# Kernel tuning notes

Measured on AMD Instinct MI355X. Metric: run time of the kernel, lower is better.

Reference implementation:

```python
import jax, jax.numpy as jnp
import numpy as np

N_TYPES = 4
D_DESC = 256
H = 256
N_ATOMS = 131072


def setup_inputs() -> dict:
    key = jax.random.key(0)
    ks = jax.random.split(key, 8)
    descriptors = jax.random.normal(ks[0], (N_ATOMS, D_DESC), dtype=jnp.float32)
    elems = jax.random.randint(ks[1], (N_ATOMS,), 0, N_TYPES, dtype=jnp.int32)
    # Per-type MLP params: stacked over the type axis T.
    s1 = 1.0 / np.sqrt(D_DESC)
    s2 = 1.0 / np.sqrt(H)
    W1 = jax.random.normal(ks[2], (N_TYPES, D_DESC, H), dtype=jnp.float32) * s1
    b1 = jnp.zeros((N_TYPES, H), dtype=jnp.float32)
    W2 = jax.random.normal(ks[3], (N_TYPES, H, H), dtype=jnp.float32) * s2
    b2 = jnp.zeros((N_TYPES, H), dtype=jnp.float32)
    W3 = jax.random.normal(ks[4], (N_TYPES, H), dtype=jnp.float32) * s2  # output dim 1, squeezed
    b3 = jnp.zeros((N_TYPES,), dtype=jnp.float32)
    return {"descriptors": descriptors, "elems": elems,
            "W1": W1, "b1": b1, "W2": W2, "b2": b2, "W3": W3, "b3": b3}


def reference(descriptors, elems, W1, b1, W2, b2, W3, b3):
    # Equivalent to: for each atom, run the MLP subnet of its element type and
    # scatter the scalar output back to the per-atom attribute vector.
    # Vectorized as batched-per-type GEMMs followed by a per-atom type gather
    # (dense dispatch: fixed shapes, jit-friendly).
    # h1: [T, N, H]
    h1 = jnp.tanh(jnp.einsum('nd,tdh->tnh', descriptors, W1) + b1[:, None, :])
    h2 = jnp.tanh(jnp.einsum('tnh,thk->tnk', h1, W2) + b2[:, None, :])
    out_t = jnp.einsum('tnh,th->tn', h2, W3) + b3[:, None]  # [T, N]
    # select per-atom row according to its element type
    per_atom = out_t[elems, jnp.arange(out_t.shape[1])]  # [N]
    return per_atom
```

## Files before the change

### kernel.cpp

```cpp
#include <hip/hip_runtime.h>
#include <hip/hip_bf16.h>
#include <stdint.h>


typedef __attribute__((ext_vector_type(8))) short short8;
typedef __attribute__((ext_vector_type(4))) float f32x4;

#define NPB 256
#define NTY 4
#define XBUF_BYTES 69632

typedef __attribute__((address_space(3))) void lds_void;
typedef __attribute__((address_space(1))) const void glb_void;

__device__ __forceinline__ unsigned short f2bf(float f) {
    union { float f; uint32_t u; } v; v.f = f;
    uint32_t u = v.u;
    uint32_t r = (u + 0x7FFFu + ((u >> 16) & 1u)) >> 16;
    return (unsigned short)r;
}
__device__ __forceinline__ float fast_tanh(float x) {
    x = fminf(fmaxf(x, -10.0f), 10.0f);
    float e = __expf(2.0f * x);
    return (e - 1.0f) * __builtin_amdgcn_rcpf(e + 1.0f);
}


__global__ void count_k(const int* __restrict__ elems, int n, int chunk,
                        int* __restrict__ counts) {
    __shared__ int h[NTY];
    if (threadIdx.x < NTY) h[threadIdx.x] = 0;
    __syncthreads();
    const int start = blockIdx.x * chunk;
    const int end   = min(start + chunk, n);
    for (int i = start + threadIdx.x; i < end; i += blockDim.x)
        atomicAdd(&h[elems[i]], 1);
    __syncthreads();
    if (threadIdx.x < NTY) counts[threadIdx.x * NPB + blockIdx.x] = h[threadIdx.x];
}

__global__ void prefix_k(const int* __restrict__ counts,
                         int* __restrict__ cursor, int* __restrict__ hdr) {
    __shared__ int tot[NTY];
    const int t = threadIdx.x;
    if (t < NTY) {
        int s = 0;
        for (int b = 0; b < NPB; ++b) s += counts[t * NPB + b];
        tot[t] = s;
    }
    __syncthreads();
    if (t == 0) {
        int b = 0, tb = 0;
        for (int ty = 0; ty < NTY; ++ty) {
            hdr[ty]      = tot[ty];
            hdr[8 + ty]  = b;
            hdr[12 + ty] = tb;
            b  += tot[ty];
            tb += (tot[ty] + 63) >> 6;
        }
        hdr[16] = tb;
    }
    __syncthreads();
    if (t < NTY) {
        int run = hdr[8 + t];
        for (int b = 0; b < NPB; ++b) {
            cursor[t * NPB + b] = run;
            run += counts[t * NPB + b];
        }
    }
}

__global__ void scatter_k(const int* __restrict__ elems, int n, int chunk,
                          const int* __restrict__ cursor, int* __restrict__ sorted) {
    __shared__ int cur[NTY];
    if (threadIdx.x < NTY) cur[threadIdx.x] = cursor[threadIdx.x * NPB + blockIdx.x];
    __syncthreads();
    const int start = blockIdx.x * chunk;
    const int end   = min(start + chunk, n);
    for (int i = start + threadIdx.x; i < end; i += blockDim.x) {
        int ty  = elems[i];
        int pos = atomicAdd(&cur[ty], 1);
        sorted[pos] = i;
    }
}

__global__ void wconv_k(const float* __restrict__ W1, const float* __restrict__ W2,
                        unsigned short* __restrict__ w1s, unsigned short* __restrict__ w2s) {
    int gid  = blockIdx.x * blockDim.x + threadIdx.x;
    int lane = gid & 63;
    int ks   = (gid >> 6) & 7;
    int tile = (gid >> 9) & 15;
    int t    = (gid >> 13) & 3;
    int layer = gid >> 15;
    const float* W = layer ? W2 : W1;
    unsigned short* o = layer ? w2s : w1s;
    int dbase = ks * 32 + ((lane >> 4) << 3);
    int col   = tile * 16 + (lane & 15);
    unsigned short v[8];
#pragma unroll
    for (int j = 0; j < 8; ++j)
        v[j] = f2bf(W[(size_t)t * 65536 + (size_t)(dbase + j) * 256 + col]);
    unsigned short* dst = o + ((size_t)(t * 16 + tile) * 8 + ks) * 512 + lane * 8;
    *(short8*)dst = *(short8*)v;
}

__device__ __forceinline__ short8 read_xfrag(const char* cb, int a, int c0) {
    const int swz = (a & 7) << 4;
    const int cs0 = c0 ^ swz;
    const int cs1 = (c0 + 16) ^ swz;
    const int ab  = (a >> 4) * 17408 + (a & 15) * 64;
    const float4 f0 = *(const float4*)(cb + ab + (cs0 >> 6) * 1088 + (cs0 & 0x30));
    const float4 f1 = *(const float4*)(cb + ab + (cs1 >> 6) * 1088 + (cs1 & 0x30));
    union { short8 s; __hip_bfloat162 h[4]; } u;
    u.h[0] = __float22bfloat162_rn(make_float2(f0.x, f0.y));
    u.h[1] = __float22bfloat162_rn(make_float2(f0.z, f0.w));
    u.h[2] = __float22bfloat162_rn(make_float2(f1.x, f1.y));
    u.h[3] = __float22bfloat162_rn(make_float2(f1.z, f1.w));
    return u.s;
}

__global__ __launch_bounds__(512, 2) void mlp_k(
    const float* __restrict__ desc,
    const float* __restrict__ b1g,
    const float* __restrict__ b2g,
    const float* __restrict__ W3,
    const float* __restrict__ b3,
    const int* __restrict__ hdr,
    const int* __restrict__ sorted,
    const unsigned short* __restrict__ w1s,
    const unsigned short* __restrict__ w2s,
    float* __restrict__ out)
{
    __shared__ __align__(16) char buf[2][XBUF_BYTES];
    __shared__ float part[8][64];

    const int tid  = threadIdx.x;
    const int lane = tid & 63;
    const int w    = tid >> 6;
    const int g    = lane >> 4;
    const int a16  = lane & 15;
    const int sa   = lane >> 2;
    const int qq   = lane & 3;
    const int gw   = w & 3;
    const int ch   = w >> 2;
    const int sswz = (sa & 7) << 4;

    const int t     = blockIdx.x >> 6;
    const int bslot = blockIdx.x & 63;
    const int cnt   = hdr[t];
    const int base  = hdr[8 + t];
    const int ntile = (cnt + 63) >> 6;
    if (bslot >= ntile) return;

#define STAGE(J, BP)                                                          \
    {                                                                         \
        const int gg_  = (J) * 64 + gw * 16 + sa;                             \
        const int idx_ = (gg_ < cnt) ? sorted[base + gg_] : 0;                \
        const float* rowp_ = desc + (size_t)idx_ * 256;                       \
        _Pragma("unroll")                                                     \
        for (int i_ = 0; i_ < 8; ++i_) {                                      \
            const int c_ = ch * 8 + i_;                                       \
            const float* src_ = rowp_ + (((c_ * 64 + qq * 16) ^ sswz) >> 2);  \
            char* dst_ = (BP) + gw * 17408 + c_ * 1088;                       \
            __builtin_amdgcn_global_load_lds((glb_void*)src_,                 \
                                             (lds_void*)dst_, 16, 0, 0);      \
        }                                                                     \
    }

    int j = bslot;
    STAGE(j, buf[0]);

    const unsigned short* w1t = w1s + (size_t)t * (16 * 8 * 512);
    const unsigned short* w2t = w2s + (size_t)t * (16 * 8 * 512);
    short8 wf1[2][8], wf2[2][8];
#pragma unroll
    for (int q = 0; q < 2; ++q)
#pragma unroll
        for (int ks = 0; ks < 8; ++ks) {
            wf1[q][ks] = *(const short8*)(w1t + ((size_t)((w * 2 + q) * 8 + ks)) * 512 + lane * 8);
            wf2[q][ks] = *(const short8*)(w2t + ((size_t)((w * 2 + q) * 8 + ks)) * 512 + lane * 8);
        }
    float4 bq[2];
    float  w3r[2], b2r[2];
#pragma unroll
    for (int q = 0; q < 2; ++q) {
        bq[q]  = *(const float4*)(b1g + t * 256 + (w * 2 + q) * 16 + g * 4);
        const int kout = (w * 2 + q) * 16 + a16;
        w3r[q] = W3[t * 256 + kout];
        b2r[q] = b2g[t * 256 + kout];
    }
    const float b3v = b3[t];

    for (int k = 0;; ++k) {
        const int cur = k & 1;
        const int jn  = j + 64;
        const bool has_next = (jn < ntile);

        asm volatile("s_waitcnt vmcnt(0)" ::: "memory");
        __syncthreads();

        if (has_next) STAGE(jn, buf[cur ^ 1]);

        const char* cb = buf[cur];

        f32x4 acc[2][4];
#pragma unroll
        for (int q = 0; q < 2; ++q)
#pragma unroll
            for (int nt = 0; nt < 4; ++nt)
                acc[q][nt] = (f32x4){0.f, 0.f, 0.f, 0.f};

#pragma unroll
        for (int ks = 0; ks < 8; ++ks) {
            short8 bh[4];
            const int c0 = ks * 128 + g * 32;
#pragma unroll
            for (int nt = 0; nt < 4; ++nt)
                bh[nt] = read_xfrag(cb, nt * 16 + a16, c0);
#pragma unroll
            for (int q = 0; q < 2; ++q)
#pragma unroll
                for (int nt = 0; nt < 4; ++nt)
                    acc[q][nt] = __builtin_amdgcn_mfma_f32_16x16x32_bf16(wf1[q][ks], bh[nt], acc[q][nt], 0, 0, 0);
        }
        __syncthreads();

        {
            char* hb = buf[cur];
#pragma unroll
            for (int q = 0; q < 2; ++q) {
                const int h0 = (w * 2 + q) * 16 + g * 4;
#pragma unroll
                for (int nt = 0; nt < 4; ++nt) {
                    const int atom = nt * 16 + a16;
                    unsigned short h4[4];
                    h4[0] = f2bf(fast_tanh(acc[q][nt][0] + bq[q].x));
                    h4[1] = f2bf(fast_tanh(acc[q][nt][1] + bq[q].y));
                    h4[2] = f2bf(fast_tanh(acc[q][nt][2] + bq[q].z));
                    h4[3] = f2bf(fast_tanh(acc[q][nt][3] + bq[q].w));
                    const int off = atom * 512 + ((h0 * 2) ^ ((atom & 7) << 4));
                    *(ushort4*)(hb + off) = *(ushort4*)h4;
                }
            }
        }
        __syncthreads();

        f32x4 acc2[4][2];
#pragma unroll
        for (int mt = 0; mt < 4; ++mt)
#pragma unroll
            for (int q = 0; q < 2; ++q)
                acc2[mt][q] = (f32x4){0.f, 0.f, 0.f, 0.f};

#pragma unroll
        for (int ks = 0; ks < 8; ++ks) {
            short8 ah[4];
            const int colb = ks * 64 + g * 16;
#pragma unroll
            for (int mt = 0; mt < 4; ++mt) {
                const int row = mt * 16 + a16;
                const int off = row * 512 + (colb ^ ((row & 7) << 4));
                ah[mt] = *(const short8*)(cb + off);
            }
#pragma unroll
            for (int mt = 0; mt < 4; ++mt)
#pragma unroll
                for (int q = 0; q < 2; ++q)
                    acc2[mt][q] = __builtin_amdgcn_mfma_f32_16x16x32_bf16(ah[mt], wf2[q][ks], acc2[mt][q], 0, 0, 0);
        }

        float psum[4][4];
#pragma unroll
        for (int mt = 0; mt < 4; ++mt)
#pragma unroll
            for (int r = 0; r < 4; ++r)
                psum[mt][r] = 0.f;

#pragma unroll
        for (int q = 0; q < 2; ++q)
#pragma unroll
            for (int mt = 0; mt < 4; ++mt)
#pragma unroll
                for (int r = 0; r < 4; ++r)
                    psum[mt][r] += fast_tanh(acc2[mt][q][r] + b2r[q]) * w3r[q];

#pragma unroll
        for (int m = 1; m <= 8; m <<= 1)
#pragma unroll
            for (int mt = 0; mt < 4; ++mt)
#pragma unroll
                for (int r = 0; r < 4; ++r)
                    psum[mt][r] += __shfl_xor(psum[mt][r], m, 64);

        if (a16 == 0) {
#pragma unroll
            for (int mt = 0; mt < 4; ++mt)
#pragma unroll
                for (int r = 0; r < 4; ++r)
                    part[w][mt * 16 + g * 4 + r] = psum[mt][r];
        }
        __syncthreads();

        if (tid < 64) {
            const int gg = j * 64 + tid;
            if (gg < cnt) {
                float v = b3v;
#pragma unroll
                for (int ww = 0; ww < 8; ++ww) v += part[ww][tid];
                out[sorted[base + gg]] = v;
            }
        }

        if (!has_next) break;
        j = jn;
    }
#undef STAGE
}

extern "C" void kernel_launch(void* const* d_in, const int* in_sizes, int n_in,
                              void* d_out, int out_size, void* d_ws, size_t ws_size,
                              hipStream_t stream) {
    const float* desc = (const float*)d_in[0];
    const int*   elems = (const int*)d_in[1];
    const float* W1 = (const float*)d_in[2];
    const float* b1 = (const float*)d_in[3];
    const float* W2 = (const float*)d_in[4];
    const float* b2 = (const float*)d_in[5];
    const float* W3 = (const float*)d_in[6];
    const float* b3 = (const float*)d_in[7];
    float* out = (float*)d_out;
    const int n = in_sizes[1];

    char* ws = (char*)d_ws;
    int* hdr    = (int*)ws;
    int* counts = (int*)(ws + 128);
    int* cursor = (int*)(ws + 128 + 4 * NPB * 4);
    int* sorted = (int*)(ws + 128 + 8 * NPB * 4);
    unsigned short* w1s = (unsigned short*)((char*)sorted + (size_t)n * 4);
    unsigned short* w2s = w1s + (size_t)4 * 16 * 8 * 512;

    const int chunk = (n + NPB - 1) / NPB;

    count_k<<<NPB, 256, 0, stream>>>(elems, n, chunk, counts);
    prefix_k<<<1, 64, 0, stream>>>(counts, cursor, hdr);
    scatter_k<<<NPB, 256, 0, stream>>>(elems, n, chunk, cursor, sorted);
    wconv_k<<<256, 256, 0, stream>>>(W1, W2, w1s, w2s);

    mlp_k<<<NTY * 64, 512, 0, stream>>>(desc, b1, b2, W3, b3,
                                        hdr, sorted, w1s, w2s, out);
}
```

Baseline: 111.9 us.

## Split MLP hidden dimension across 16 waves per block instead of 8

Doubles the block to 1024 threads so each of 16 waves owns a single 16-column slice of the hidden dimension, halving per-wave weight registers and MFMA accumulators. Staging loads and the final cross-wave reduction are widened to match. The aim is more waves in flight per CU to hide LDS and global latency. The cost is one block per CU, more barrier participants and a longer reduction over 16 partials. Each wave also re-reads the same X fragments per MFMA, so LDS traffic per FLOP doubles.

```diff
diff --git a/kernel.cpp b/kernel.cpp
--- a/kernel.cpp
+++ b/kernel.cpp
@@ -119,7 +119,7 @@
     return u.s;
 }
 
-__global__ __launch_bounds__(512, 2) void mlp_k(
+__global__ __launch_bounds__(1024, 1) void mlp_k(
     const float* __restrict__ desc,
     const float* __restrict__ b1g,
     const float* __restrict__ b2g,
@@ -132,7 +132,7 @@
     float* __restrict__ out)
 {
     __shared__ __align__(16) char buf[2][XBUF_BYTES];
-    __shared__ float part[8][64];
+    __shared__ float part[16][64];
 
     const int tid  = threadIdx.x;
     const int lane = tid & 63;
@@ -158,8 +158,8 @@
         const int idx_ = (gg_ < cnt) ? sorted[base + gg_] : 0;                \
         const float* rowp_ = desc + (size_t)idx_ * 256;                       \
         _Pragma("unroll")                                                     \
-        for (int i_ = 0; i_ < 8; ++i_) {                                      \
-            const int c_ = ch * 8 + i_;                                       \
+        for (int i_ = 0; i_ < 4; ++i_) {                                      \
+            const int c_ = ch * 4 + i_;                                       \
             const float* src_ = rowp_ + (((c_ * 64 + qq * 16) ^ sswz) >> 2);  \
             char* dst_ = (BP) + gw * 17408 + c_ * 1088;                       \
             __builtin_amdgcn_global_load_lds((glb_void*)src_,                 \
@@ -172,23 +172,16 @@
 
     const unsigned short* w1t = w1s + (size_t)t * (16 * 8 * 512);
     const unsigned short* w2t = w2s + (size_t)t * (16 * 8 * 512);
-    short8 wf1[2][8], wf2[2][8];
-#pragma unroll
-    for (int q = 0; q < 2; ++q)
-#pragma unroll
-        for (int ks = 0; ks < 8; ++ks) {
-            wf1[q][ks] = *(const short8*)(w1t + ((size_t)((w * 2 + q) * 8 + ks)) * 512 + lane * 8);
-            wf2[q][ks] = *(const short8*)(w2t + ((size_t)((w * 2 + q) * 8 + ks)) * 512 + lane * 8);
-        }
-    float4 bq[2];
-    float  w3r[2], b2r[2];
-#pragma unroll
-    for (int q = 0; q < 2; ++q) {
-        bq[q]  = *(const float4*)(b1g + t * 256 + (w * 2 + q) * 16 + g * 4);
-        const int kout = (w * 2 + q) * 16 + a16;
-        w3r[q] = W3[t * 256 + kout];
-        b2r[q] = b2g[t * 256 + kout];
-    }
+    short8 wf1[8], wf2[8];
+#pragma unroll
+    for (int ks = 0; ks < 8; ++ks) {
+        wf1[ks] = *(const short8*)(w1t + ((size_t)(w * 8 + ks)) * 512 + lane * 8);
+        wf2[ks] = *(const short8*)(w2t + ((size_t)(w * 8 + ks)) * 512 + lane * 8);
+    }
+    const float4 bq = *(const float4*)(b1g + t * 256 + w * 16 + g * 4);
+    const int kout  = w * 16 + a16;
+    const float w3r = W3[t * 256 + kout];
+    const float b2r = b2g[t * 256 + kout];
     const float b3v = b3[t];
 
     for (int k = 0;; ++k) {
@@ -203,12 +196,10 @@
 
         const char* cb = buf[cur];
 
-        f32x4 acc[2][4];
-#pragma unroll
-        for (int q = 0; q < 2; ++q)
-#pragma unroll
-            for (int nt = 0; nt < 4; ++nt)
-                acc[q][nt] = (f32x4){0.f, 0.f, 0.f, 0.f};
+        f32x4 acc[4];
+#pragma unroll
+        for (int nt = 0; nt < 4; ++nt)
+            acc[nt] = (f32x4){0.f, 0.f, 0.f, 0.f};
 
 #pragma unroll
         for (int ks = 0; ks < 8; ++ks) {
@@ -218,39 +209,32 @@
             for (int nt = 0; nt < 4; ++nt)
                 bh[nt] = read_xfrag(cb, nt * 16 + a16, c0);
 #pragma unroll
-            for (int q = 0; q < 2; ++q)
-#pragma unroll
-                for (int nt = 0; nt < 4; ++nt)
-                    acc[q][nt] = __builtin_amdgcn_mfma_f32_16x16x32_bf16(wf1[q][ks], bh[nt], acc[q][nt], 0, 0, 0);
+            for (int nt = 0; nt < 4; ++nt)
+                acc[nt] = __builtin_amdgcn_mfma_f32_16x16x32_bf16(wf1[ks], bh[nt], acc[nt], 0, 0, 0);
         }
         __syncthreads();
 
         {
             char* hb = buf[cur];
-#pragma unroll
-            for (int q = 0; q < 2; ++q) {
-                const int h0 = (w * 2 + q) * 16 + g * 4;
-#pragma unroll
-                for (int nt = 0; nt < 4; ++nt) {
-                    const int atom = nt * 16 + a16;
-                    unsigned short h4[4];
-                    h4[0] = f2bf(fast_tanh(acc[q][nt][0] + bq[q].x));
-                    h4[1] = f2bf(fast_tanh(acc[q][nt][1] + bq[q].y));
-                    h4[2] = f2bf(fast_tanh(acc[q][nt][2] + bq[q].z));
-                    h4[3] = f2bf(fast_tanh(acc[q][nt][3] + bq[q].w));
-                    const int off = atom * 512 + ((h0 * 2) ^ ((atom & 7) << 4));
-                    *(ushort4*)(hb + off) = *(ushort4*)h4;
-                }
+            const int h0 = w * 16 + g * 4;
+#pragma unroll
+            for (int nt = 0; nt < 4; ++nt) {
+                const int atom = nt * 16 + a16;
+                unsigned short h4[4];
+                h4[0] = f2bf(fast_tanh(acc[nt][0] + bq.x));
+                h4[1] = f2bf(fast_tanh(acc[nt][1] + bq.y));
+                h4[2] = f2bf(fast_tanh(acc[nt][2] + bq.z));
+                h4[3] = f2bf(fast_tanh(acc[nt][3] + bq.w));
+                const int off = atom * 512 + ((h0 * 2) ^ ((atom & 7) << 4));
+                *(ushort4*)(hb + off) = *(ushort4*)h4;
             }
         }
         __syncthreads();
 
-        f32x4 acc2[4][2];
+        f32x4 acc2[4];
 #pragma unroll
         for (int mt = 0; mt < 4; ++mt)
-#pragma unroll
-            for (int q = 0; q < 2; ++q)
-                acc2[mt][q] = (f32x4){0.f, 0.f, 0.f, 0.f};
+            acc2[mt] = (f32x4){0.f, 0.f, 0.f, 0.f};
 
 #pragma unroll
         for (int ks = 0; ks < 8; ++ks) {
@@ -264,9 +248,7 @@
             }
 #pragma unroll
             for (int mt = 0; mt < 4; ++mt)
-#pragma unroll
-                for (int q = 0; q < 2; ++q)
-                    acc2[mt][q] = __builtin_amdgcn_mfma_f32_16x16x32_bf16(ah[mt], wf2[q][ks], acc2[mt][q], 0, 0, 0);
+                acc2[mt] = __builtin_amdgcn_mfma_f32_16x16x32_bf16(ah[mt], wf2[ks], acc2[mt], 0, 0, 0);
         }
 
         float psum[4][4];
@@ -274,15 +256,7 @@
         for (int mt = 0; mt < 4; ++mt)
 #pragma unroll
             for (int r = 0; r < 4; ++r)
-                psum[mt][r] = 0.f;
-
-#pragma unroll
-        for (int q = 0; q < 2; ++q)
-#pragma unroll
-            for (int mt = 0; mt < 4; ++mt)
-#pragma unroll
-                for (int r = 0; r < 4; ++r)
-                    psum[mt][r] += fast_tanh(acc2[mt][q][r] + b2r[q]) * w3r[q];
+                psum[mt][r] = fast_tanh(acc2[mt][r] + b2r) * w3r;
 
 #pragma unroll
         for (int m = 1; m <= 8; m <<= 1)
@@ -306,7 +280,7 @@
             if (gg < cnt) {
                 float v = b3v;
 #pragma unroll
-                for (int ww = 0; ww < 8; ++ww) v += part[ww][tid];
+                for (int ww = 0; ww < 16; ++ww) v += part[ww][tid];
                 out[sorted[base + gg]] = v;
             }
         }
@@ -346,6 +320,6 @@
     scatter_k<<<NPB, 256, 0, stream>>>(elems, n, chunk, cursor, sorted);
     wconv_k<<<256, 256, 0, stream>>>(W1, W2, w1s, w2s);
 
-    mlp_k<<<NTY * 64, 512, 0, stream>>>(desc, b1, b2, W3, b3,
-                                        hdr, sorted, w1s, w2s, out);
-}
+    mlp_k<<<NTY * 64, 1024, 0, stream>>>(desc, b1, b2, W3, b3,
+                                         hdr, sorted, w1s, w2s, out);
+}
```

Result: slower. 178.3 us (+59.3%).
